# Performance work log

Measured on AMD Instinct MI355X. Metric: run time of the kernel, lower is better.

The kernel has to match this reference:

```python
import math
import jax, jax.numpy as jnp
import numpy as np

H = 8
DIM = 256
HD = DIM // H
SCALE = math.sqrt(HD)
EPS = 1e-16


def _segment_softmax(scores, dst, num_nodes):
    # scores: [E, H], dst: [E] -> softmax over edges sharing the same dst
    m = jax.ops.segment_max(scores, dst, num_segments=num_nodes)  # [N, H]
    m = jnp.where(jnp.isfinite(m), m, 0.0)  # empty segments -> -inf -> 0
    e = jnp.exp(scores - m[dst])
    s = jax.ops.segment_sum(e, dst, num_segments=num_nodes)  # [N, H]
    return e / (s[dst] + EPS)


def _graph_attention(x, edges, wq, bq, wk, bk, wv, bv, wo, bo):
    # x: [N, DIM]; edges: [2, E] (src, dst). Dropout is identity (eval mode).
    N = x.shape[0]
    Q = (x @ wq + bq).reshape(N, H, HD)
    K = (x @ wk + bk).reshape(N, H, HD)
    V = (x @ wv + bv).reshape(N, H, HD)
    src, dst = edges[0], edges[1]
    scores = jnp.einsum('ehd,ehd->eh', Q[dst], K[src]) / SCALE  # [E, H]
    attn = _segment_softmax(scores, dst, N)  # [E, H]
    msgs = V[src] * attn[:, :, None]  # [E, H, HD]
    out = jax.ops.segment_sum(msgs, dst, num_segments=N).reshape(N, DIM)
    return out @ wo + bo


def _linear_params(key, fan_in, fan_out):
    k1, k2 = jax.random.split(key)
    bound = 1.0 / math.sqrt(fan_in)
    w = jax.random.uniform(k1, (fan_in, fan_out), minval=-bound, maxval=bound, dtype=jnp.float32)
    b = jax.random.uniform(k2, (fan_out,), minval=-bound, maxval=bound, dtype=jnp.float32)
    return w, b


def setup_inputs() -> dict:
    key = jax.random.key(0)
    ks = jax.random.split(key, 12)
    n_slot, n_dom = 20000, 1000
    e_slot, e_dom = 320000, 16000
    inp = {
        'slot_x': jax.random.normal(ks[0], (n_slot, DIM), dtype=jnp.float32),
        'domain_x': jax.random.normal(ks[1], (n_dom, DIM), dtype=jnp.float32),
        'slot_edges': jax.random.randint(ks[2], (2, e_slot), 0, n_slot, dtype=jnp.int32),
        'domain_edges': jax.random.randint(ks[3], (2, e_dom), 0, n_dom, dtype=jnp.int32),
    }
    names = ['wq', 'wk', 'wv', 'wo']
    for i, nm in enumerate(names):
        w, b = _linear_params(ks[4 + i], DIM, DIM)
        inp[f'slot_{nm}'] = w
        inp[f'slot_{nm}_b'] = b
    for i, nm in enumerate(names):
        w, b = _linear_params(ks[8 + i], DIM, DIM)
        inp[f'dom_{nm}'] = w
        inp[f'dom_{nm}_b'] = b
    return inp


def reference(slot_x, domain_x, slot_edges, domain_edges,
              slot_wq, slot_wq_b, slot_wk, slot_wk_b, slot_wv, slot_wv_b, slot_wo, slot_wo_b,
              dom_wq, dom_wq_b, dom_wk, dom_wk_b, dom_wv, dom_wv_b, dom_wo, dom_wo_b):
    # slot branch: self-attention on slot graph + identity residual
    slot_out = _graph_attention(slot_x, slot_edges,
                                slot_wq, slot_wq_b, slot_wk, slot_wk_b,
                                slot_wv, slot_wv_b, slot_wo, slot_wo_b) + slot_x
    # domain branch
    dom_out = _graph_attention(domain_x, domain_edges,
                               dom_wq, dom_wq_b, dom_wk, dom_wk_b,
                               dom_wv, dom_wv_b, dom_wo, dom_wo_b) + domain_x
    return slot_out, dom_out
```

## Files before the change

kernel.cpp:

```cpp
#include <hip/hip_runtime.h>
#include <hip/hip_bf16.h>

#define DIM 256
#define INV_SCALE 0.17677669529663687f
#define SM_EPS 1e-16f
#define BM 128
#define BN 64
#define BK 32

typedef unsigned short ushortT;
typedef unsigned int uintT;
typedef __attribute__((ext_vector_type(8))) __bf16 bf16x8;
typedef __attribute__((ext_vector_type(4))) float f32x4;

__device__ __forceinline__ float bf2f(ushortT u) {
    return __uint_as_float(((uintT)u) << 16);
}
__device__ __forceinline__ ushortT f2bf(float f) {
    uintT u = __float_as_uint(f);
    u += 0x7FFFu + ((u >> 16) & 1u);
    return (ushortT)(u >> 16);
}

struct WPack { const void* w[8]; const void* b[8]; };

__global__ void sniff_kernel(const ushortT* __restrict__ x, int* __restrict__ flag) {
    int lane = threadIdx.x & 63;
    ushortT u = x[lane * 2];
    int e = (u >> 7) & 0xFF;
    bool sane = ((u & 0x7FFFu) == 0) || (e >= 0x66 && e <= 0x90);
    unsigned long long m = __ballot(sane);
    if (lane == 0) *flag = (__popcll(m) >= 32) ? 1 : 0;
}

__global__ __launch_bounds__(256) void prep_kernel(
        const void* __restrict__ xs, const void* __restrict__ xd,
        ushortT* __restrict__ xbs, ushortT* __restrict__ xbd,
        int* __restrict__ cs, int* __restrict__ cd,
        int n4s, int n4d, int Ns_, int Nd_, const int* __restrict__ flag) {
    const int y = blockIdx.y;
    int i = blockIdx.x * 256 + threadIdx.x;
    if (y >= 2) {
        int N = (y == 3) ? Nd_ : Ns_;
        int* c = (y == 3) ? cd : cs;
        if (i < N) c[i] = 0;
        return;
    }
    const int n4 = y ? n4d : n4s;
    if (i >= n4) return;
    const void* x = y ? xd : xs;
    ushortT* xb = y ? xbd : xbs;
    if (*flag) {
        ((ushort4*)xb)[i] = ((const ushort4*)x)[i];
    } else {
        float4 v = ((const float4*)x)[i];
        ushort4 o;
        o.x = f2bf(v.x); o.y = f2bf(v.y); o.z = f2bf(v.z); o.w = f2bf(v.w);
        ((ushort4*)xb)[i] = o;
    }
}

__global__ __launch_bounds__(256) void convw_kernel(WPack pk,
                                                    ushortT* __restrict__ wT,
                                                    float* __restrict__ biasF,
                                                    const int* __restrict__ flag) {
    const int which = blockIdx.y;
    const bool m16 = (*flag != 0);
    if (blockIdx.x == 256) {
        const void* b = pk.b[which];
        int i = threadIdx.x;
        float v = m16 ? bf2f(((const ushortT*)b)[i]) : ((const float*)b)[i];
        biasF[which * 256 + i] = v;
    } else {
        const void* w = pk.w[which];
        int n = blockIdx.x, k = threadIdx.x;
        float v = m16 ? bf2f(((const ushortT*)w)[k * 256 + n])
                      : ((const float*)w)[k * 256 + n];
        wT[(size_t)which * 65536 + n * 256 + k] = f2bf(v);
    }
}

__global__ __launch_bounds__(256) void csr_count2(const int* __restrict__ ds,
                                                  const int* __restrict__ dd,
                                                  int* __restrict__ cs, int* __restrict__ cd,
                                                  int Es, int Ed) {
    const int y = blockIdx.y;
    int E = y ? Ed : Es;
    int e = blockIdx.x * 256 + threadIdx.x;
    if (e >= E) return;
    const int* dst = y ? dd : ds;
    int* c = y ? cd : cs;
    atomicAdd(&c[dst[e]], 1);
}
__global__ __launch_bounds__(256) void scan_bsum2(const int* __restrict__ cs,
                                                  const int* __restrict__ cd,
                                                  int* __restrict__ bss, int* __restrict__ bsd,
                                                  int Ns_, int Nd_) {
    __shared__ int sh[256];
    const int y = blockIdx.y;
    int N = y ? Nd_ : Ns_;
    const int* c = y ? cd : cs;
    int* bs = y ? bsd : bss;
    int t = threadIdx.x, i = blockIdx.x * 256 + t;
    sh[t] = (i < N) ? c[i] : 0;
    __syncthreads();
    #pragma unroll
    for (int off = 128; off > 0; off >>= 1) {
        if (t < off) sh[t] += sh[t + off];
        __syncthreads();
    }
    if (t == 0) bs[blockIdx.x] = sh[0];
}
__global__ __launch_bounds__(256) void scan_boff2(int* __restrict__ bss, int* __restrict__ bsd,
                                                  int nbs_, int nbd_) {
    __shared__ int sh[256];
    const int y = blockIdx.y;
    int nb = y ? nbd_ : nbs_;
    int* bs = y ? bsd : bss;
    int t = threadIdx.x;
    sh[t] = (t < nb) ? bs[t] : 0;
    __syncthreads();
    for (int off = 1; off < 256; off <<= 1) {
        int v = (t >= off) ? sh[t - off] : 0;
        __syncthreads();
        sh[t] += v;
        __syncthreads();
    }
    if (t < nb) bs[t] = (t == 0) ? 0 : sh[t - 1];
}
__global__ __launch_bounds__(256) void scan_write2(const int* __restrict__ cs,
                                                   const int* __restrict__ cd,
                                                   const int* __restrict__ bss,
                                                   const int* __restrict__ bsd,
                                                   int* __restrict__ rps, int* __restrict__ rpd,
                                                   int* __restrict__ curs, int* __restrict__ curd,
                                                   int Ns_, int Nd_) {
    __shared__ int sh[256];
    const int y = blockIdx.y;
    int N = y ? Nd_ : Ns_;
    const int* c = y ? cd : cs;
    const int* bo = y ? bsd : bss;
    int* rp = y ? rpd : rps;
    int* cur = y ? curd : curs;
    int t = threadIdx.x, i = blockIdx.x * 256 + t;
    int v = (i < N) ? c[i] : 0;
    sh[t] = v;
    __syncthreads();
    for (int off = 1; off < 256; off <<= 1) {
        int u = (t >= off) ? sh[t - off] : 0;
        __syncthreads();
        sh[t] += u;
        __syncthreads();
    }
    int excl = bo[blockIdx.x] + ((t == 0) ? 0 : sh[t - 1]);
    if (i < N) {
        rp[i] = excl;
        cur[i] = excl;
        if (i == N - 1) rp[N] = excl + v;
    }
}
__global__ __launch_bounds__(256) void csr_scatter2(const int* __restrict__ ss,
                                                    const int* __restrict__ ds,
                                                    const int* __restrict__ sd,
                                                    const int* __restrict__ dd,
                                                    int* __restrict__ curs, int* __restrict__ curd,
                                                    int* __restrict__ cols, int* __restrict__ cold,
                                                    int Es, int Ed) {
    const int y = blockIdx.y;
    int E = y ? Ed : Es;
    int e = blockIdx.x * 256 + threadIdx.x;
    if (e >= E) return;
    const int* src = y ? sd : ss;
    const int* dst = y ? dd : ds;
    int* cur = y ? curd : curs;
    int* col = y ? cold : cols;
    int pos = atomicAdd(&cur[dst[e]], 1);
    col[pos] = src[e];
}

__device__ __forceinline__ void gemm_core(const ushortT* __restrict__ A,
                                          const ushortT* __restrict__ BT,
                                          int row0, int col0, int M,
                                          f32x4 (&acc)[2][4]) {
    __shared__ ushortT As[BM * BK];
    __shared__ ushortT Bs[BN * BK];
    const int tid  = threadIdx.x;
    const int wid  = tid >> 6;
    const int lane = tid & 63;
    const int r_i = tid >> 2;
    const int kq8 = (tid & 3) << 3;
    const int m   = lane & 15;
    const int q   = lane >> 4;

    const size_t rA0 = (size_t)min(row0 + r_i, M - 1) * DIM;
    const size_t rA1 = (size_t)min(row0 + 64 + r_i, M - 1) * DIM;
    const size_t rB  = (size_t)(col0 + r_i) * DIM;

    for (int k0 = 0; k0 < DIM; k0 += BK) {
        uint4 a0v = *(const uint4*)(A + rA0 + k0 + kq8);
        uint4 a1v = *(const uint4*)(A + rA1 + k0 + kq8);
        uint4 bv  = *(const uint4*)(BT + rB + k0 + kq8);
        __syncthreads();
        *(uint4*)&As[r_i * BK + kq8]        = a0v;
        *(uint4*)&As[(64 + r_i) * BK + kq8] = a1v;
        *(uint4*)&Bs[r_i * BK + kq8]        = bv;
        __syncthreads();

        bf16x8 af0 = *(const bf16x8*)&As[(wid * 32 + m) * BK + q * 8];
        bf16x8 af1 = *(const bf16x8*)&As[(wid * 32 + 16 + m) * BK + q * 8];
        #pragma unroll
        for (int j = 0; j < 4; ++j) {
            bf16x8 bf = *(const bf16x8*)&Bs[(j * 16 + m) * BK + q * 8];
            acc[0][j] = __builtin_amdgcn_mfma_f32_16x16x32_bf16(af0, bf, acc[0][j], 0, 0, 0);
            acc[1][j] = __builtin_amdgcn_mfma_f32_16x16x32_bf16(af1, bf, acc[1][j], 0, 0, 0);
        }
    }
}

__global__ __launch_bounds__(256) void gemm_qkv(
        const ushortT* __restrict__ As_, const ushortT* __restrict__ Ad_,
        const ushortT* __restrict__ wT, const float* __restrict__ biasF,
        ushortT* __restrict__ Cs, ushortT* __restrict__ Cd,
        size_t zss, size_t zsd, int Ms, int Md, int nbs)
{
    const int z = blockIdx.z;
    const bool dom = (int)blockIdx.x >= nbs;
    const int bx = dom ? blockIdx.x - nbs : blockIdx.x;
    const ushortT* A = dom ? Ad_ : As_;
    const int M = dom ? Md : Ms;
    const int widx = z + (dom ? 4 : 0);
    const ushortT* BT = wT + (size_t)widx * 65536;
    const float* bias = biasF + widx * 256;
    ushortT* C = (dom ? Cd : Cs) + (size_t)z * (dom ? zsd : zss);

    const int row0 = bx * BM;
    const int col0 = blockIdx.y * BN;
    const int wid = threadIdx.x >> 6, lane = threadIdx.x & 63;
    const int m = lane & 15, q = lane >> 4;

    f32x4 acc[2][4];
    #pragma unroll
    for (int i = 0; i < 2; ++i)
        #pragma unroll
        for (int j = 0; j < 4; ++j) acc[i][j] = (f32x4){0.f, 0.f, 0.f, 0.f};

    gemm_core(A, BT, row0, col0, M, acc);

    #pragma unroll
    for (int i = 0; i < 2; ++i)
        #pragma unroll
        for (int j = 0; j < 4; ++j) {
            const int col = col0 + j * 16 + m;
            const float bval = bias[col];
            #pragma unroll
            for (int r = 0; r < 4; ++r) {
                const int row = row0 + wid * 32 + i * 16 + q * 4 + r;
                if (row < M)
                    C[(size_t)row * DIM + col] = f2bf(acc[i][j][r] + bval);
            }
        }
}

__global__ __launch_bounds__(256) void gemm_out(
        const ushortT* __restrict__ As_, const ushortT* __restrict__ Ad_,
        const ushortT* __restrict__ wT, const float* __restrict__ biasF,
        const void* __restrict__ xs, const void* __restrict__ xd,
        void* __restrict__ dout, int Ms, int Md, int nbs,
        const int* __restrict__ flag)
{
    const bool dom = (int)blockIdx.x >= nbs;
    const int bx = dom ? blockIdx.x - nbs : blockIdx.x;
    const ushortT* A = dom ? Ad_ : As_;
    const int M = dom ? Md : Ms;
    const int widx = 3 + (dom ? 4 : 0);
    const ushortT* BT = wT + (size_t)widx * 65536;
    const float* bias = biasF + widx * 256;
    const void* res = dom ? xd : xs;
    const size_t outOff = dom ? (size_t)Ms * DIM : 0;

    const int row0 = bx * BM;
    const int col0 = blockIdx.y * BN;
    const int wid = threadIdx.x >> 6, lane = threadIdx.x & 63;
    const int m = lane & 15, q = lane >> 4;

    f32x4 acc[2][4];
    #pragma unroll
    for (int i = 0; i < 2; ++i)
        #pragma unroll
        for (int j = 0; j < 4; ++j) acc[i][j] = (f32x4){0.f, 0.f, 0.f, 0.f};

    gemm_core(A, BT, row0, col0, M, acc);

    const bool m16 = (*flag != 0);
    #pragma unroll
    for (int i = 0; i < 2; ++i)
        #pragma unroll
        for (int j = 0; j < 4; ++j) {
            const int col = col0 + j * 16 + m;
            const float bval = bias[col];
            #pragma unroll
            for (int r = 0; r < 4; ++r) {
                const int row = row0 + wid * 32 + i * 16 + q * 4 + r;
                if (row < M) {
                    const size_t ridx = (size_t)row * DIM + col;
                    float v = acc[i][j][r] + bval;
                    v += m16 ? bf2f(((const ushortT*)res)[ridx])
                             : ((const float*)res)[ridx];
                    if (m16) ((ushortT*)dout)[outOff + ridx] = f2bf(v);
                    else     ((float*)dout)[outOff + ridx] = v;
                }
            }
        }
}

__global__ __launch_bounds__(256) void attn_kernel(
        const ushortT* __restrict__ Qs, const ushortT* __restrict__ Ks,
        const ushortT* __restrict__ Vs, const int* __restrict__ rps,
        const int* __restrict__ css, ushortT* __restrict__ aggs,
        const ushortT* __restrict__ Qd_, const ushortT* __restrict__ Kd_,
        const ushortT* __restrict__ Vd_, const int* __restrict__ rpd,
        const int* __restrict__ csd, ushortT* __restrict__ aggd,
        int Ns_, int Ntot)
{
    const int g = blockIdx.x * 4 + (threadIdx.x >> 6);
    if (g >= Ntot) return;
    const bool dom = g >= Ns_;
    const int d = dom ? g - Ns_ : g;
    const int t = threadIdx.x & 63;
    const ushortT* Qb = dom ? Qd_ : Qs;
    const ushortT* Kb = dom ? Kd_ : Ks;
    const ushortT* Vb = dom ? Vd_ : Vs;
    const int* rowptr = dom ? rpd : rps;
    const int* colsrc = dom ? csd : css;
    ushortT* aggb = dom ? aggd : aggs;

    const int t4 = t * 4;
    const size_t cbase = (size_t)d * DIM + t4;
    uint2 qv = *(const uint2*)(Qb + cbase);
    const float q0 = bf2f((ushortT)(qv.x & 0xFFFF)), q1 = bf2f((ushortT)(qv.x >> 16));
    const float q2 = bf2f((ushortT)(qv.y & 0xFFFF)), q3 = bf2f((ushortT)(qv.y >> 16));

    float a0 = 0.f, a1 = 0.f, a2 = 0.f, a3 = 0.f, den = 0.f;

    auto PROC = [&](uint2 kvc, uint2 vvc) {
        float k0 = bf2f((ushortT)(kvc.x & 0xFFFF)), k1 = bf2f((ushortT)(kvc.x >> 16));
        float k2 = bf2f((ushortT)(kvc.y & 0xFFFF)), k3 = bf2f((ushortT)(kvc.y >> 16));
        float p = q0 * k0 + q1 * k1 + q2 * k2 + q3 * k3;
        p += __shfl_xor(p, 1, 8);
        p += __shfl_xor(p, 2, 8);
        p += __shfl_xor(p, 4, 8);
        const float w = __expf(fminf(p * INV_SCALE, 60.0f));
        den += w;
        a0 += w * bf2f((ushortT)(vvc.x & 0xFFFF));
        a1 += w * bf2f((ushortT)(vvc.x >> 16));
        a2 += w * bf2f((ushortT)(vvc.y & 0xFFFF));
        a3 += w * bf2f((ushortT)(vvc.y >> 16));
    };

    const int beg = rowptr[d], end = rowptr[d + 1];
    int i = beg;
    for (; i + 4 <= end; i += 4) {
        const int s0 = colsrc[i], s1 = colsrc[i + 1];
        const int s2 = colsrc[i + 2], s3 = colsrc[i + 3];
        const size_t b0 = (size_t)s0 * DIM + t4, b1 = (size_t)s1 * DIM + t4;
        const size_t b2 = (size_t)s2 * DIM + t4, b3 = (size_t)s3 * DIM + t4;
        uint2 k0v = *(const uint2*)(Kb + b0), v0v = *(const uint2*)(Vb + b0);
        uint2 k1v = *(const uint2*)(Kb + b1), v1v = *(const uint2*)(Vb + b1);
        uint2 k2v = *(const uint2*)(Kb + b2), v2v = *(const uint2*)(Vb + b2);
        uint2 k3v = *(const uint2*)(Kb + b3), v3v = *(const uint2*)(Vb + b3);
        PROC(k0v, v0v); PROC(k1v, v1v); PROC(k2v, v2v); PROC(k3v, v3v);
    }
    for (; i < end; ++i) {
        const size_t sb = (size_t)colsrc[i] * DIM + t4;
        uint2 kv = *(const uint2*)(Kb + sb);
        uint2 vv = *(const uint2*)(Vb + sb);
        PROC(kv, vv);
    }

    const float r = 1.0f / (den + SM_EPS);
    ushort4 o;
    o.x = f2bf(a0 * r); o.y = f2bf(a1 * r); o.z = f2bf(a2 * r); o.w = f2bf(a3 * r);
    *(ushort4*)(aggb + cbase) = o;
}

extern "C" void kernel_launch(void* const* d_in, const int* in_sizes, int n_in,
                              void* d_out, int out_size, void* d_ws, size_t ws_size,
                              hipStream_t stream)
{
    const void* slot_x = d_in[0];
    const void* dom_x  = d_in[1];
    const int* slot_edges = (const int*)d_in[2];
    const int* dom_edges  = (const int*)d_in[3];
    const int Ns = in_sizes[0] / DIM;
    const int Nd = in_sizes[1] / DIM;
    const int Es = in_sizes[2] / 2;
    const int Ed = in_sizes[3] / 2;

    WPack pk;
    for (int i = 0; i < 8; ++i) { pk.w[i] = d_in[4 + 2 * i]; pk.b[i] = d_in[5 + 2 * i]; }

    char* p = (char*)d_ws;
    size_t o = 0;
    auto take = [&](size_t b) { void* r = p + o; o = (o + b + 255) & ~(size_t)255; return r; };
    const size_t ndS = (size_t)Ns * DIM;
    const size_t ndD = (size_t)Nd * DIM;
    ushortT* xb_s  = (ushortT*)take(ndS * 2);
    ushortT* qkv_s = (ushortT*)take(3 * ndS * 2);
    ushortT* agg_s = (ushortT*)take(ndS * 2);
    ushortT* xb_d  = (ushortT*)take(ndD * 2);
    ushortT* qkv_d = (ushortT*)take(3 * ndD * 2);
    ushortT* agg_d = (ushortT*)take(ndD * 2);
    ushortT* wT    = (ushortT*)take(8 * 65536 * 2);
    float*   biasF = (float*)take(8 * 256 * 4);
    int* rp_s  = (int*)take((size_t)(Ns + 1) * 4);
    int* cur_s = (int*)take((size_t)Ns * 4);
    int* cnt_s = (int*)take((size_t)Ns * 4);
    int* bs_s  = (int*)take(256 * 4);
    int* col_s = (int*)take((size_t)Es * 4);
    int* rp_d  = (int*)take((size_t)(Nd + 1) * 4);
    int* cur_d = (int*)take((size_t)Nd * 4);
    int* cnt_d = (int*)take((size_t)Nd * 4);
    int* bs_d  = (int*)take(256 * 4);
    int* col_d = (int*)take((size_t)Ed * 4);
    int* flag  = (int*)(p + ws_size - 256);

    const int* src_s = slot_edges;
    const int* dst_s = slot_edges + Es;
    const int* src_d = dom_edges;
    const int* dst_d = dom_edges + Ed;

    const int n4s = Ns * DIM / 4, n4d = Nd * DIM / 4;
    const int nbN = (Ns + 255) / 256;
    const int nbE = (Es + 255) / 256;
    const int nbs = (Ns + BM - 1) / BM;
    const int nbd = (Nd + BM - 1) / BM;

    hipLaunchKernelGGL(sniff_kernel, dim3(1), dim3(64), 0, stream,
                       (const ushortT*)slot_x, flag);
    hipLaunchKernelGGL(prep_kernel, dim3((n4s + 255) / 256, 4), dim3(256), 0, stream,
                       slot_x, dom_x, xb_s, xb_d, cnt_s, cnt_d,
                       n4s, n4d, Ns, Nd, flag);
    hipLaunchKernelGGL(convw_kernel, dim3(257, 8), dim3(256), 0, stream,
                       pk, wT, biasF, flag);

    hipLaunchKernelGGL(csr_count2, dim3(nbE, 2), dim3(256), 0, stream,
                       dst_s, dst_d, cnt_s, cnt_d, Es, Ed);
    hipLaunchKernelGGL(scan_bsum2, dim3(nbN, 2), dim3(256), 0, stream,
                       cnt_s, cnt_d, bs_s, bs_d, Ns, Nd);
    hipLaunchKernelGGL(scan_boff2, dim3(1, 2), dim3(256), 0, stream,
                       bs_s, bs_d, nbN, (Nd + 255) / 256);
    hipLaunchKernelGGL(scan_write2, dim3(nbN, 2), dim3(256), 0, stream,
                       cnt_s, cnt_d, bs_s, bs_d, rp_s, rp_d, cur_s, cur_d, Ns, Nd);
    hipLaunchKernelGGL(csr_scatter2, dim3(nbE, 2), dim3(256), 0, stream,
                       src_s, dst_s, src_d, dst_d, cur_s, cur_d, col_s, col_d, Es, Ed);

    hipLaunchKernelGGL(gemm_qkv, dim3(nbs + nbd, DIM / BN, 3), dim3(256), 0, stream,
                       xb_s, xb_d, wT, biasF, qkv_s, qkv_d, ndS, ndD, Ns, Nd, nbs);

    const int Ntot = Ns + Nd;
    hipLaunchKernelGGL(attn_kernel, dim3((Ntot + 3) / 4), dim3(256), 0, stream,
                       qkv_s, qkv_s + ndS, qkv_s + 2 * ndS, rp_s, col_s, agg_s,
                       qkv_d, qkv_d + ndD, qkv_d + 2 * ndD, rp_d, col_d, agg_d,
                       Ns, Ntot);

    hipLaunchKernelGGL(gemm_out, dim3(nbs + nbd, DIM / BN), dim3(256), 0, stream,
                       agg_s, agg_d, wT, biasF, slot_x, dom_x, d_out, Ns, Nd, nbs, flag);
}
```

Before: 264.5 us.

## Merge prep, CSR build and QKV GEMM into fewer launches with decoupled-lookback scan

```diff
diff --git a/kernel.cpp b/kernel.cpp
--- a/kernel.cpp
+++ b/kernel.cpp
@@ -24,158 +24,74 @@
 
 struct WPack { const void* w[8]; const void* b[8]; };
 
-__global__ void sniff_kernel(const ushortT* __restrict__ x, int* __restrict__ flag) {
+__device__ __forceinline__ bool sniff_m16(const ushortT* __restrict__ x) {
     int lane = threadIdx.x & 63;
     ushortT u = x[lane * 2];
     int e = (u >> 7) & 0xFF;
     bool sane = ((u & 0x7FFFu) == 0) || (e >= 0x66 && e <= 0x90);
     unsigned long long m = __ballot(sane);
-    if (lane == 0) *flag = (__popcll(m) >= 32) ? 1 : 0;
-}
-
-__global__ __launch_bounds__(256) void prep_kernel(
+    return __popcll(m) >= 32;
+}
+
+__global__ __launch_bounds__(256) void megaA(
         const void* __restrict__ xs, const void* __restrict__ xd,
-        ushortT* __restrict__ xbs, ushortT* __restrict__ xbd,
-        int* __restrict__ cs, int* __restrict__ cd,
-        int n4s, int n4d, int Ns_, int Nd_, const int* __restrict__ flag) {
-    const int y = blockIdx.y;
-    int i = blockIdx.x * 256 + threadIdx.x;
-    if (y >= 2) {
-        int N = (y == 3) ? Nd_ : Ns_;
-        int* c = (y == 3) ? cd : cs;
-        if (i < N) c[i] = 0;
-        return;
-    }
-    const int n4 = y ? n4d : n4s;
-    if (i >= n4) return;
-    const void* x = y ? xd : xs;
-    ushortT* xb = y ? xbd : xbs;
-    if (*flag) {
-        ((ushort4*)xb)[i] = ((const ushort4*)x)[i];
+        const ushortT* __restrict__ sniff_src,
+        ushortT* __restrict__ xb_s, ushortT* __restrict__ xb_d,
+        WPack pk, ushortT* __restrict__ wT, float* __restrict__ biasF,
+        int* __restrict__ cnt_s, int* __restrict__ cnt_d,
+        uintT* __restrict__ st_s, uintT* __restrict__ st_d,
+        int* __restrict__ done, int* __restrict__ flagWs,
+        int n4s, int n4d, int Ns_, int Nd_, int nbN_, int nbD_,
+        int nA0, int nA1, int nA2)
+{
+    const bool m16 = sniff_m16(sniff_src);
+    const int bid = blockIdx.x;
+    const int t = threadIdx.x;
+
+    if (bid < nA0 + nA1) {
+        const bool d = bid >= nA0;
+        const int li = d ? bid - nA0 : bid;
+        const int n4 = d ? n4d : n4s;
+        const int i = li * 256 + t;
+        if (i >= n4) return;
+        const void* x = d ? xd : xs;
+        ushortT* xb = d ? xb_d : xb_s;
+        if (m16) {
+            ((ushort4*)xb)[i] = ((const ushort4*)x)[i];
+        } else {
+            float4 v = ((const float4*)x)[i];
+            ushort4 o2;
+            o2.x = f2bf(v.x); o2.y = f2bf(v.y); o2.z = f2bf(v.z); o2.w = f2bf(v.w);
+            ((ushort4*)xb)[i] = o2;
+        }
+    } else if (bid < nA0 + nA1 + nA2) {
+        const int r = bid - (nA0 + nA1);
+        const int which = r / 257;
+        const int j = r % 257;
+        if (j == 256) {
+            const void* b = pk.b[which];
+            float v = m16 ? bf2f(((const ushortT*)b)[t]) : ((const float*)b)[t];
+            biasF[which * 256 + t] = v;
+        } else {
+            const void* w = pk.w[which];
+            float v = m16 ? bf2f(((const ushortT*)w)[t * 256 + j])
+                          : ((const float*)w)[t * 256 + j];
+            wT[(size_t)which * 65536 + j * 256 + t] = f2bf(v);
+        }
     } else {
-        float4 v = ((const float4*)x)[i];
-        ushort4 o;
-        o.x = f2bf(v.x); o.y = f2bf(v.y); o.z = f2bf(v.z); o.w = f2bf(v.w);
-        ((ushort4*)xb)[i] = o;
-    }
-}
-
-__global__ __launch_bounds__(256) void convw_kernel(WPack pk,
-                                                    ushortT* __restrict__ wT,
-                                                    float* __restrict__ biasF,
-                                                    const int* __restrict__ flag) {
-    const int which = blockIdx.y;
-    const bool m16 = (*flag != 0);
-    if (blockIdx.x == 256) {
-        const void* b = pk.b[which];
-        int i = threadIdx.x;
-        float v = m16 ? bf2f(((const ushortT*)b)[i]) : ((const float*)b)[i];
-        biasF[which * 256 + i] = v;
-    } else {
-        const void* w = pk.w[which];
-        int n = blockIdx.x, k = threadIdx.x;
-        float v = m16 ? bf2f(((const ushortT*)w)[k * 256 + n])
-                      : ((const float*)w)[k * 256 + n];
-        wT[(size_t)which * 65536 + n * 256 + k] = f2bf(v);
-    }
-}
-
-__global__ __launch_bounds__(256) void csr_count2(const int* __restrict__ ds,
-                                                  const int* __restrict__ dd,
-                                                  int* __restrict__ cs, int* __restrict__ cd,
-                                                  int Es, int Ed) {
-    const int y = blockIdx.y;
-    int E = y ? Ed : Es;
-    int e = blockIdx.x * 256 + threadIdx.x;
-    if (e >= E) return;
-    const int* dst = y ? dd : ds;
-    int* c = y ? cd : cs;
-    atomicAdd(&c[dst[e]], 1);
-}
-__global__ __launch_bounds__(256) void scan_bsum2(const int* __restrict__ cs,
-                                                  const int* __restrict__ cd,
-                                                  int* __restrict__ bss, int* __restrict__ bsd,
-                                                  int Ns_, int Nd_) {
-    __shared__ int sh[256];
-    const int y = blockIdx.y;
-    int N = y ? Nd_ : Ns_;
-    const int* c = y ? cd : cs;
-    int* bs = y ? bsd : bss;
-    int t = threadIdx.x, i = blockIdx.x * 256 + t;
-    sh[t] = (i < N) ? c[i] : 0;
-    __syncthreads();
-    #pragma unroll
-    for (int off = 128; off > 0; off >>= 1) {
-        if (t < off) sh[t] += sh[t + off];
-        __syncthreads();
-    }
-    if (t == 0) bs[blockIdx.x] = sh[0];
-}
-__global__ __launch_bounds__(256) void scan_boff2(int* __restrict__ bss, int* __restrict__ bsd,
-                                                  int nbs_, int nbd_) {
-    __shared__ int sh[256];
-    const int y = blockIdx.y;
-    int nb = y ? nbd_ : nbs_;
-    int* bs = y ? bsd : bss;
-    int t = threadIdx.x;
-    sh[t] = (t < nb) ? bs[t] : 0;
-    __syncthreads();
-    for (int off = 1; off < 256; off <<= 1) {
-        int v = (t >= off) ? sh[t - off] : 0;
-        __syncthreads();
-        sh[t] += v;
-        __syncthreads();
-    }
-    if (t < nb) bs[t] = (t == 0) ? 0 : sh[t - 1];
-}
-__global__ __launch_bounds__(256) void scan_write2(const int* __restrict__ cs,
-                                                   const int* __restrict__ cd,
-                                                   const int* __restrict__ bss,
-                                                   const int* __restrict__ bsd,
-                                                   int* __restrict__ rps, int* __restrict__ rpd,
-                                                   int* __restrict__ curs, int* __restrict__ curd,
-                                                   int Ns_, int Nd_) {
-    __shared__ int sh[256];
-    const int y = blockIdx.y;
-    int N = y ? Nd_ : Ns_;
-    const int* c = y ? cd : cs;
-    const int* bo = y ? bsd : bss;
-    int* rp = y ? rpd : rps;
-    int* cur = y ? curd : curs;
-    int t = threadIdx.x, i = blockIdx.x * 256 + t;
-    int v = (i < N) ? c[i] : 0;
-    sh[t] = v;
-    __syncthreads();
-    for (int off = 1; off < 256; off <<= 1) {
-        int u = (t >= off) ? sh[t - off] : 0;
-        __syncthreads();
-        sh[t] += u;
-        __syncthreads();
-    }
-    int excl = bo[blockIdx.x] + ((t == 0) ? 0 : sh[t - 1]);
-    if (i < N) {
-        rp[i] = excl;
-        cur[i] = excl;
-        if (i == N - 1) rp[N] = excl + v;
-    }
-}
-__global__ __launch_bounds__(256) void csr_scatter2(const int* __restrict__ ss,
-                                                    const int* __restrict__ ds,
-                                                    const int* __restrict__ sd,
-                                                    const int* __restrict__ dd,
-                                                    int* __restrict__ curs, int* __restrict__ curd,
-                                                    int* __restrict__ cols, int* __restrict__ cold,
-                                                    int Es, int Ed) {
-    const int y = blockIdx.y;
-    int E = y ? Ed : Es;
-    int e = blockIdx.x * 256 + threadIdx.x;
-    if (e >= E) return;
-    const int* src = y ? sd : ss;
-    const int* dst = y ? dd : ds;
-    int* cur = y ? curd : curs;
-    int* col = y ? cold : cols;
-    int pos = atomicAdd(&cur[dst[e]], 1);
-    col[pos] = src[e];
+        const int li = bid - (nA0 + nA1 + nA2);
+        const int idx = li * 256 + t;
+        if (idx < Ns_) { cnt_s[idx] = 0; return; }
+        int k = idx - Ns_;
+        if (k < Nd_) { cnt_d[k] = 0; return; }
+        k -= Nd_;
+        if (k < nbN_) { st_s[k] = 0; return; }
+        k -= nbN_;
+        if (k < nbD_) { st_d[k] = 0; return; }
+        k -= nbD_;
+        if (k == 0) *done = 0;
+        else if (k == 1) *flagWs = m16 ? 1 : 0;
+    }
 }
 
 __device__ __forceinline__ void gemm_core(const ushortT* __restrict__ A,
@@ -217,24 +133,37 @@
     }
 }
 
-__global__ __launch_bounds__(256) void gemm_qkv(
-        const ushortT* __restrict__ As_, const ushortT* __restrict__ Ad_,
+__global__ __launch_bounds__(256) void megaB(
+        const ushortT* __restrict__ xb_s, const ushortT* __restrict__ xb_d,
         const ushortT* __restrict__ wT, const float* __restrict__ biasF,
-        ushortT* __restrict__ Cs, ushortT* __restrict__ Cd,
-        size_t zss, size_t zsd, int Ms, int Md, int nbs)
+        ushortT* __restrict__ qkv_s, ushortT* __restrict__ qkv_d,
+        size_t zss, size_t zsd, int Ms, int Md, int nbs_, int nbq_,
+        const int* __restrict__ dst_s, const int* __restrict__ dst_d,
+        int* __restrict__ cnt_s, int* __restrict__ cnt_d, int Es_, int Ed_)
 {
-    const int z = blockIdx.z;
-    const bool dom = (int)blockIdx.x >= nbs;
-    const int bx = dom ? blockIdx.x - nbs : blockIdx.x;
-    const ushortT* A = dom ? Ad_ : As_;
+    const int bid = blockIdx.x;
+    const int nq = nbq_ * 12;
+    if (bid >= nq) {
+        const int idx = (bid - nq) * 256 + threadIdx.x;
+        if (idx < Es_) atomicAdd(&cnt_s[dst_s[idx]], 1);
+        else { int e = idx - Es_; if (e < Ed_) atomicAdd(&cnt_d[dst_d[e]], 1); }
+        return;
+    }
+    const int z  = bid / (nbq_ * 4);
+    const int r  = bid % (nbq_ * 4);
+    const int by = r / nbq_;
+    const int bx0 = r % nbq_;
+    const bool dom = bx0 >= nbs_;
+    const int bx = dom ? bx0 - nbs_ : bx0;
+    const ushortT* A = dom ? xb_d : xb_s;
     const int M = dom ? Md : Ms;
     const int widx = z + (dom ? 4 : 0);
     const ushortT* BT = wT + (size_t)widx * 65536;
     const float* bias = biasF + widx * 256;
-    ushortT* C = (dom ? Cd : Cs) + (size_t)z * (dom ? zsd : zss);
+    ushortT* C = (dom ? qkv_d : qkv_s) + (size_t)z * (dom ? zsd : zss);
 
     const int row0 = bx * BM;
-    const int col0 = blockIdx.y * BN;
+    const int col0 = by * BN;
     const int wid = threadIdx.x >> 6, lane = threadIdx.x & 63;
     const int m = lane & 15, q = lane >> 4;
 
@@ -253,12 +182,185 @@
             const int col = col0 + j * 16 + m;
             const float bval = bias[col];
             #pragma unroll
-            for (int r = 0; r < 4; ++r) {
-                const int row = row0 + wid * 32 + i * 16 + q * 4 + r;
+            for (int rr = 0; rr < 4; ++rr) {
+                const int row = row0 + wid * 32 + i * 16 + q * 4 + rr;
                 if (row < M)
-                    C[(size_t)row * DIM + col] = f2bf(acc[i][j][r] + bval);
+                    C[(size_t)row * DIM + col] = f2bf(acc[i][j][rr] + bval);
             }
         }
+}
+
+__device__ __forceinline__ uintT spack(uintT st, uintT v) { return (st << 30) | v; }
+
+__global__ __launch_bounds__(256) void scan_scatter(
+        const int* __restrict__ cnt_s, const int* __restrict__ cnt_d,
+        uintT* __restrict__ st_s, uintT* __restrict__ st_d,
+        int* __restrict__ rp_s, int* __restrict__ rp_d,
+        int* __restrict__ cur_s, int* __restrict__ cur_d,
+        int* __restrict__ done,
+        const int* __restrict__ ss, const int* __restrict__ ds,
+        const int* __restrict__ sd, const int* __restrict__ dd,
+        int* __restrict__ col_s, int* __restrict__ col_d,
+        int Ns_, int Nd_, int nbN_, int nbD_, int Es_, int Ed_)
+{
+    __shared__ int sh[256];
+    __shared__ int exclS;
+    const int b = blockIdx.x;
+    const int t = threadIdx.x;
+    const bool dom = b >= nbN_;
+    const int lb = dom ? b - nbN_ : b;
+    const int N = dom ? Nd_ : Ns_;
+    const int* cnt = dom ? cnt_d : cnt_s;
+    uintT* st = dom ? st_d : st_s;
+    int* rp = dom ? rp_d : rp_s;
+    int* cur = dom ? cur_d : cur_s;
+
+    const int i = lb * 256 + t;
+    const int v = (i < N) ? cnt[i] : 0;
+    sh[t] = v;
+    __syncthreads();
+    for (int off = 1; off < 256; off <<= 1) {
+        int u = (t >= off) ? sh[t - off] : 0;
+        __syncthreads();
+        sh[t] += u;
+        __syncthreads();
+    }
+
+    if (t == 0) {
+        const uintT agg = (uintT)sh[255];
+        uintT excl = 0;
+        if (lb == 0) {
+            __hip_atomic_store(&st[0], spack(2u, agg), __ATOMIC_RELEASE,
+                               __HIP_MEMORY_SCOPE_AGENT);
+        } else {
+            __hip_atomic_store(&st[lb], spack(1u, agg), __ATOMIC_RELEASE,
+                               __HIP_MEMORY_SCOPE_AGENT);
+            int j = lb - 1;
+            while (j >= 0) {
+                uintT s = __hip_atomic_load(&st[j], __ATOMIC_ACQUIRE,
+                                            __HIP_MEMORY_SCOPE_AGENT);
+                uintT tag = s >> 30;
+                if (tag == 2u) { excl += s & 0x3FFFFFFFu; break; }
+                if (tag == 1u) { excl += s & 0x3FFFFFFFu; --j; }
+            }
+            __hip_atomic_store(&st[lb], spack(2u, excl + agg), __ATOMIC_RELEASE,
+                               __HIP_MEMORY_SCOPE_AGENT);
+        }
+        exclS = (int)excl;
+    }
+    __syncthreads();
+    const int excl = exclS;
+    if (i < N) {
+        const int e = excl + ((t == 0) ? 0 : sh[t - 1]);
+        rp[i] = e;
+        cur[i] = e;
+        if (i == N - 1) rp[N] = e + v;
+    }
+
+    __threadfence();
+    __syncthreads();
+    if (t == 0) {
+        __hip_atomic_fetch_add(done, 1, __ATOMIC_ACQ_REL, __HIP_MEMORY_SCOPE_AGENT);
+        const int nb = nbN_ + nbD_;
+        while (__hip_atomic_load(done, __ATOMIC_ACQUIRE, __HIP_MEMORY_SCOPE_AGENT) < nb) {}
+    }
+    __syncthreads();
+
+    const int total = Es_ + Ed_;
+    const int stride = (nbN_ + nbD_) * 256;
+    for (int idx = b * 256 + t; idx < total; idx += stride) {
+        if (idx < Es_) {
+            int pos = atomicAdd(&cur_s[ds[idx]], 1);
+            col_s[pos] = ss[idx];
+        } else {
+            int e = idx - Es_;
+            int pos = atomicAdd(&cur_d[dd[e]], 1);
+            col_d[pos] = sd[e];
+        }
+    }
+}
+
+__global__ __launch_bounds__(256) void attn_kernel(
+        const ushortT* __restrict__ Qs, const ushortT* __restrict__ Ks,
+        const ushortT* __restrict__ Vs, const int* __restrict__ rps,
+        const int* __restrict__ css, ushortT* __restrict__ aggs,
+        const ushortT* __restrict__ Qd_, const ushortT* __restrict__ Kd_,
+        const ushortT* __restrict__ Vd_, const int* __restrict__ rpd,
+        const int* __restrict__ csd, ushortT* __restrict__ aggd,
+        int Ns_, int Ntot)
+{
+    const int sub = threadIdx.x & 31;
+    const int g = blockIdx.x * 8 + (threadIdx.x >> 5);
+    if (g >= Ntot) return;
+    const bool dom = g >= Ns_;
+    const int d = dom ? g - Ns_ : g;
+    const ushortT* Qb = dom ? Qd_ : Qs;
+    const ushortT* Kb = dom ? Kd_ : Ks;
+    const ushortT* Vb = dom ? Vd_ : Vs;
+    const int* rowptr = dom ? rpd : rps;
+    const int* colsrc = dom ? csd : css;
+    ushortT* aggb = dom ? aggd : aggs;
+
+    const int c8 = sub * 8;
+    const size_t cbase = (size_t)d * DIM + c8;
+
+    uint4 qv = *(const uint4*)(Qb + cbase);
+    float qf[8];
+    qf[0] = bf2f((ushortT)(qv.x & 0xFFFF)); qf[1] = bf2f((ushortT)(qv.x >> 16));
+    qf[2] = bf2f((ushortT)(qv.y & 0xFFFF)); qf[3] = bf2f((ushortT)(qv.y >> 16));
+    qf[4] = bf2f((ushortT)(qv.z & 0xFFFF)); qf[5] = bf2f((ushortT)(qv.z >> 16));
+    qf[6] = bf2f((ushortT)(qv.w & 0xFFFF)); qf[7] = bf2f((ushortT)(qv.w >> 16));
+
+    float acc[8] = {};
+    float den = 0.f;
+
+    auto PROC = [&](uint4 kv, uint4 vv) {
+        float kf[8];
+        kf[0] = bf2f((ushortT)(kv.x & 0xFFFF)); kf[1] = bf2f((ushortT)(kv.x >> 16));
+        kf[2] = bf2f((ushortT)(kv.y & 0xFFFF)); kf[3] = bf2f((ushortT)(kv.y >> 16));
+        kf[4] = bf2f((ushortT)(kv.z & 0xFFFF)); kf[5] = bf2f((ushortT)(kv.z >> 16));
+        kf[6] = bf2f((ushortT)(kv.w & 0xFFFF)); kf[7] = bf2f((ushortT)(kv.w >> 16));
+        float p = qf[0] * kf[0] + qf[1] * kf[1] + qf[2] * kf[2] + qf[3] * kf[3]
+                + qf[4] * kf[4] + qf[5] * kf[5] + qf[6] * kf[6] + qf[7] * kf[7];
+        p += __shfl_xor(p, 1, 4);
+        p += __shfl_xor(p, 2, 4);
+        const float w = __expf(fminf(p * INV_SCALE, 60.0f));
+        den += w;
+        acc[0] += w * bf2f((ushortT)(vv.x & 0xFFFF));
+        acc[1] += w * bf2f((ushortT)(vv.x >> 16));
+        acc[2] += w * bf2f((ushortT)(vv.y & 0xFFFF));
+        acc[3] += w * bf2f((ushortT)(vv.y >> 16));
+        acc[4] += w * bf2f((ushortT)(vv.z & 0xFFFF));
+        acc[5] += w * bf2f((ushortT)(vv.z >> 16));
+        acc[6] += w * bf2f((ushortT)(vv.w & 0xFFFF));
+        acc[7] += w * bf2f((ushortT)(vv.w >> 16));
+    };
+
+    const int beg = rowptr[d], end = rowptr[d + 1];
+    int i = beg;
+    for (; i + 4 <= end; i += 4) {
+        const int s0 = colsrc[i], s1 = colsrc[i + 1];
+        const int s2 = colsrc[i + 2], s3 = colsrc[i + 3];
+        const size_t b0 = (size_t)s0 * DIM + c8, b1 = (size_t)s1 * DIM + c8;
+        const size_t b2 = (size_t)s2 * DIM + c8, b3 = (size_t)s3 * DIM + c8;
+        uint4 k0v = *(const uint4*)(Kb + b0), v0v = *(const uint4*)(Vb + b0);
+        uint4 k1v = *(const uint4*)(Kb + b1), v1v = *(const uint4*)(Vb + b1);
+        uint4 k2v = *(const uint4*)(Kb + b2), v2v = *(const uint4*)(Vb + b2);
+        uint4 k3v = *(const uint4*)(Kb + b3), v3v = *(const uint4*)(Vb + b3);
+        PROC(k0v, v0v); PROC(k1v, v1v); PROC(k2v, v2v); PROC(k3v, v3v);
+    }
+    for (; i < end; ++i) {
+        const size_t sb = (size_t)colsrc[i] * DIM + c8;
+        PROC(*(const uint4*)(Kb + sb), *(const uint4*)(Vb + sb));
+    }
+
+    const float r = 1.0f / (den + SM_EPS);
+    uint4 o;
+    o.x = (uintT)f2bf(acc[0] * r) | ((uintT)f2bf(acc[1] * r) << 16);
+    o.y = (uintT)f2bf(acc[2] * r) | ((uintT)f2bf(acc[3] * r) << 16);
+    o.z = (uintT)f2bf(acc[4] * r) | ((uintT)f2bf(acc[5] * r) << 16);
+    o.w = (uintT)f2bf(acc[6] * r) | ((uintT)f2bf(acc[7] * r) << 16);
+    *(uint4*)(aggb + cbase) = o;
 }
 
 __global__ __launch_bounds__(256) void gemm_out(
@@ -313,76 +415,6 @@
         }
 }
 
-__global__ __launch_bounds__(256) void attn_kernel(
-        const ushortT* __restrict__ Qs, const ushortT* __restrict__ Ks,
-        const ushortT* __restrict__ Vs, const int* __restrict__ rps,
-        const int* __restrict__ css, ushortT* __restrict__ aggs,
-        const ushortT* __restrict__ Qd_, const ushortT* __restrict__ Kd_,
-        const ushortT* __restrict__ Vd_, const int* __restrict__ rpd,
-        const int* __restrict__ csd, ushortT* __restrict__ aggd,
-        int Ns_, int Ntot)
-{
-    const int g = blockIdx.x * 4 + (threadIdx.x >> 6);
-    if (g >= Ntot) return;
-    const bool dom = g >= Ns_;
-    const int d = dom ? g - Ns_ : g;
-    const int t = threadIdx.x & 63;
-    const ushortT* Qb = dom ? Qd_ : Qs;
-    const ushortT* Kb = dom ? Kd_ : Ks;
-    const ushortT* Vb = dom ? Vd_ : Vs;
-    const int* rowptr = dom ? rpd : rps;
-    const int* colsrc = dom ? csd : css;
-    ushortT* aggb = dom ? aggd : aggs;
-
-    const int t4 = t * 4;
-    const size_t cbase = (size_t)d * DIM + t4;
-    uint2 qv = *(const uint2*)(Qb + cbase);
-    const float q0 = bf2f((ushortT)(qv.x & 0xFFFF)), q1 = bf2f((ushortT)(qv.x >> 16));
-    const float q2 = bf2f((ushortT)(qv.y & 0xFFFF)), q3 = bf2f((ushortT)(qv.y >> 16));
-
-    float a0 = 0.f, a1 = 0.f, a2 = 0.f, a3 = 0.f, den = 0.f;
-
-    auto PROC = [&](uint2 kvc, uint2 vvc) {
-        float k0 = bf2f((ushortT)(kvc.x & 0xFFFF)), k1 = bf2f((ushortT)(kvc.x >> 16));
-        float k2 = bf2f((ushortT)(kvc.y & 0xFFFF)), k3 = bf2f((ushortT)(kvc.y >> 16));
-        float p = q0 * k0 + q1 * k1 + q2 * k2 + q3 * k3;
-        p += __shfl_xor(p, 1, 8);
-        p += __shfl_xor(p, 2, 8);
-        p += __shfl_xor(p, 4, 8);
-        const float w = __expf(fminf(p * INV_SCALE, 60.0f));
-        den += w;
-        a0 += w * bf2f((ushortT)(vvc.x & 0xFFFF));
-        a1 += w * bf2f((ushortT)(vvc.x >> 16));
-        a2 += w * bf2f((ushortT)(vvc.y & 0xFFFF));
-        a3 += w * bf2f((ushortT)(vvc.y >> 16));
-    };
-
-    const int beg = rowptr[d], end = rowptr[d + 1];
-    int i = beg;
-    for (; i + 4 <= end; i += 4) {
-        const int s0 = colsrc[i], s1 = colsrc[i + 1];
-        const int s2 = colsrc[i + 2], s3 = colsrc[i + 3];
-        const size_t b0 = (size_t)s0 * DIM + t4, b1 = (size_t)s1 * DIM + t4;
-        const size_t b2 = (size_t)s2 * DIM + t4, b3 = (size_t)s3 * DIM + t4;
-        uint2 k0v = *(const uint2*)(Kb + b0), v0v = *(const uint2*)(Vb + b0);
-        uint2 k1v = *(const uint2*)(Kb + b1), v1v = *(const uint2*)(Vb + b1);
-        uint2 k2v = *(const uint2*)(Kb + b2), v2v = *(const uint2*)(Vb + b2);
-        uint2 k3v = *(const uint2*)(Kb + b3), v3v = *(const uint2*)(Vb + b3);
-        PROC(k0v, v0v); PROC(k1v, v1v); PROC(k2v, v2v); PROC(k3v, v3v);
-    }
-    for (; i < end; ++i) {
-        const size_t sb = (size_t)colsrc[i] * DIM + t4;
-        uint2 kv = *(const uint2*)(Kb + sb);
-        uint2 vv = *(const uint2*)(Vb + sb);
-        PROC(kv, vv);
-    }
-
-    const float r = 1.0f / (den + SM_EPS);
-    ushort4 o;
-    o.x = f2bf(a0 * r); o.y = f2bf(a1 * r); o.z = f2bf(a2 * r); o.w = f2bf(a3 * r);
-    *(ushort4*)(aggb + cbase) = o;
-}
-
 extern "C" void kernel_launch(void* const* d_in, const int* in_sizes, int n_in,
                               void* d_out, int out_size, void* d_ws, size_t ws_size,
                               hipStream_t stream)
@@ -415,14 +447,15 @@
     int* rp_s  = (int*)take((size_t)(Ns + 1) * 4);
     int* cur_s = (int*)take((size_t)Ns * 4);
     int* cnt_s = (int*)take((size_t)Ns * 4);
-    int* bs_s  = (int*)take(256 * 4);
     int* col_s = (int*)take((size_t)Es * 4);
     int* rp_d  = (int*)take((size_t)(Nd + 1) * 4);
     int* cur_d = (int*)take((size_t)Nd * 4);
     int* cnt_d = (int*)take((size_t)Nd * 4);
-    int* bs_d  = (int*)take(256 * 4);
     int* col_d = (int*)take((size_t)Ed * 4);
-    int* flag  = (int*)(p + ws_size - 256);
+    uintT* st_s = (uintT*)take(512 * 4);
+    uintT* st_d = (uintT*)take(256 * 4);
+    int* done   = (int*)take(256);
+    int* flagWs = (int*)take(256);
 
     const int* src_s = slot_edges;
     const int* dst_s = slot_edges + Es;
@@ -431,38 +464,37 @@
 
     const int n4s = Ns * DIM / 4, n4d = Nd * DIM / 4;
     const int nbN = (Ns + 255) / 256;
-    const int nbE = (Es + 255) / 256;
+    const int nbD = (Nd + 255) / 256;
     const int nbs = (Ns + BM - 1) / BM;
     const int nbd = (Nd + BM - 1) / BM;
-
-    hipLaunchKernelGGL(sniff_kernel, dim3(1), dim3(64), 0, stream,
-                       (const ushortT*)slot_x, flag);
-    hipLaunchKernelGGL(prep_kernel, dim3((n4s + 255) / 256, 4), dim3(256), 0, stream,
-                       slot_x, dom_x, xb_s, xb_d, cnt_s, cnt_d,
-                       n4s, n4d, Ns, Nd, flag);
-    hipLaunchKernelGGL(convw_kernel, dim3(257, 8), dim3(256), 0, stream,
-                       pk, wT, biasF, flag);
-
-    hipLaunchKernelGGL(csr_count2, dim3(nbE, 2), dim3(256), 0, stream,
-                       dst_s, dst_d, cnt_s, cnt_d, Es, Ed);
-    hipLaunchKernelGGL(scan_bsum2, dim3(nbN, 2), dim3(256), 0, stream,
-                       cnt_s, cnt_d, bs_s, bs_d, Ns, Nd);
-    hipLaunchKernelGGL(scan_boff2, dim3(1, 2), dim3(256), 0, stream,
-                       bs_s, bs_d, nbN, (Nd + 255) / 256);
-    hipLaunchKernelGGL(scan_write2, dim3(nbN, 2), dim3(256), 0, stream,
-                       cnt_s, cnt_d, bs_s, bs_d, rp_s, rp_d, cur_s, cur_d, Ns, Nd);
-    hipLaunchKernelGGL(csr_scatter2, dim3(nbE, 2), dim3(256), 0, stream,
-                       src_s, dst_s, src_d, dst_d, cur_s, cur_d, col_s, col_d, Es, Ed);
-
-    hipLaunchKernelGGL(gemm_qkv, dim3(nbs + nbd, DIM / BN, 3), dim3(256), 0, stream,
-                       xb_s, xb_d, wT, biasF, qkv_s, qkv_d, ndS, ndD, Ns, Nd, nbs);
+    const int nbq = nbs + nbd;
+
+    const int nA0 = (n4s + 255) / 256;
+    const int nA1 = (n4d + 255) / 256;
+    const int nA2 = 257 * 8;
+    const int nZ  = (Ns + Nd + nbN + nbD + 2 + 255) / 256;
+    hipLaunchKernelGGL(megaA, dim3(nA0 + nA1 + nA2 + nZ), dim3(256), 0, stream,
+                       slot_x, dom_x, (const ushortT*)slot_x, xb_s, xb_d,
+                       pk, wT, biasF, cnt_s, cnt_d, st_s, st_d, done, flagWs,
+                       n4s, n4d, Ns, Nd, nbN, nbD, nA0, nA1, nA2);
+
+    const int nCnt = (Es + Ed + 255) / 256;
+    hipLaunchKernelGGL(megaB, dim3(nbq * 12 + nCnt), dim3(256), 0, stream,
+                       xb_s, xb_d, wT, biasF, qkv_s, qkv_d, ndS, ndD,
+                       Ns, Nd, nbs, nbq, dst_s, dst_d, cnt_s, cnt_d, Es, Ed);
+
+    hipLaunchKernelGGL(scan_scatter, dim3(nbN + nbD), dim3(256), 0, stream,
+                       cnt_s, cnt_d, st_s, st_d, rp_s, rp_d, cur_s, cur_d, done,
+                       src_s, dst_s, src_d, dst_d, col_s, col_d,
+                       Ns, Nd, nbN, nbD, Es, Ed);
 
     const int Ntot = Ns + Nd;
-    hipLaunchKernelGGL(attn_kernel, dim3((Ntot + 3) / 4), dim3(256), 0, stream,
+    hipLaunchKernelGGL(attn_kernel, dim3((Ntot + 7) / 8), dim3(256), 0, stream,
                        qkv_s, qkv_s + ndS, qkv_s + 2 * ndS, rp_s, col_s, agg_s,
                        qkv_d, qkv_d + ndD, qkv_d + 2 * ndD, rp_d, col_d, agg_d,
                        Ns, Ntot);
 
-    hipLaunchKernelGGL(gemm_out, dim3(nbs + nbd, DIM / BN), dim3(256), 0, stream,
-                       agg_s, agg_d, wT, biasF, slot_x, dom_x, d_out, Ns, Nd, nbs, flag);
-}
+    hipLaunchKernelGGL(gemm_out, dim3(nbq, DIM / BN), dim3(256), 0, stream,
+                       agg_s, agg_d, wT, biasF, slot_x, dom_x, d_out,
+                       Ns, Nd, nbs, flagWs);
+}
```

New measurement: 271.5 us. +2.6%, slower.
